# Performance work log

Measured on AMD Instinct MI355X. Metric: run time of the kernel, lower is better.

Reference implementation:

```python
import jax, jax.numpy as jnp
import numpy as np

N_NODES = 100000
N_EDGES = 6400000
EPS = 1e-12


def _gcn_conv(x, edge_index, W, b, n):
    # PyG GCNConv(normalize=True): add self-loops, symmetric deg^-1/2 norm
    src, dst = edge_index[0], edge_index[1]
    loop = jnp.arange(n)
    row = jnp.concatenate([src, loop])
    col = jnp.concatenate([dst, loop])
    deg = jax.ops.segment_sum(jnp.ones(row.shape[0], dtype=x.dtype), col, num_segments=n)
    dinv = jnp.where(deg > 0, jax.lax.rsqrt(deg), 0.0)
    norm = dinv[row] * dinv[col]                       # [E+N]
    xw = x @ W                                          # [N,16]
    out = jax.ops.segment_sum(xw[row] * norm[:, None], col, num_segments=n)
    return out + b


def _sage_conv(x, edge_index, Wl, bl, Wr, n):
    # PyG SAGEConv(aggr='mean', root_weight=True, normalize=True)
    src, dst = edge_index[0], edge_index[1]
    deg = jax.ops.segment_sum(jnp.ones(src.shape[0], dtype=x.dtype), dst, num_segments=n)
    agg = jax.ops.segment_sum(x[src], dst, num_segments=n) / jnp.maximum(deg, 1.0)[:, None]
    out = agg @ Wl + bl + x @ Wr
    nrm = jnp.sqrt(jnp.sum(out * out, axis=-1, keepdims=True))
    return out / jnp.maximum(nrm, EPS)                  # F.normalize(p=2)


def setup_inputs() -> dict:
    key = jax.random.key(0)
    ks = jax.random.split(key, 16)
    s16, s128 = 1.0 / np.sqrt(16.0), 1.0 / np.sqrt(128.0)
    inp = {
        "x": jax.random.normal(ks[0], (N_NODES, 16), dtype=jnp.float32),
        "edge_index": jax.random.randint(ks[1], (2, N_EDGES), 0, N_NODES, dtype=jnp.int64),
        "W_gcn": jax.random.uniform(ks[2], (16, 16), jnp.float32, -s16, s16),
        "b_gcn": jnp.zeros((16,), jnp.float32),
        "Wl1": jax.random.uniform(ks[3], (16, 16), jnp.float32, -s16, s16),
        "bl1": jnp.zeros((16,), jnp.float32),
        "Wr1": jax.random.uniform(ks[4], (16, 16), jnp.float32, -s16, s16),
        "Wl2": jax.random.uniform(ks[5], (16, 16), jnp.float32, -s16, s16),
        "bl2": jnp.zeros((16,), jnp.float32),
        "Wr2": jax.random.uniform(ks[6], (16, 16), jnp.float32, -s16, s16),
        "W1": jax.random.uniform(ks[7], (16, 128), jnp.float32, -s16, s16),
        "b1": jax.random.uniform(ks[8], (128,), jnp.float32, -s16, s16),
        "W2": jax.random.uniform(ks[9], (128, 128), jnp.float32, -s128, s128),
        "b2": jax.random.uniform(ks[10], (128,), jnp.float32, -s128, s128),
        "W3": jax.random.uniform(ks[11], (128, 1), jnp.float32, -s128, s128),
        "b3": jax.random.uniform(ks[12], (1,), jnp.float32, -s128, s128),
    }
    return inp


def reference(x, edge_index, W_gcn, b_gcn, Wl1, bl1, Wr1, Wl2, bl2, Wr2, W1, b1, W2, b2, W3, b3):
    n = x.shape[0]
    h = jnp.tanh(_gcn_conv(x, edge_index, W_gcn, b_gcn, n))
    h = jnp.tanh(_sage_conv(h, edge_index, Wl1, bl1, Wr1, n))
    h = _sage_conv(h, edge_index, Wl2, bl2, Wr2, n)
    h = jax.nn.relu(h @ W1 + b1)
    h = jax.nn.relu(h @ W2 + b2)
    return h @ W3 + b3
```

## Files before the change

kernel.cpp:

```cpp
#include <hip/hip_runtime.h>
#include <hip/hip_bf16.h>
#include <math.h>

#define NBLK 512
#define ROWS (NBLK / 256)
#define MAXNC 512
#define STAGE_CAP 12512

__global__ void k_hist(const int* __restrict__ dst, int* __restrict__ hist,
                       int nE, int nc, int chunk) {
    __shared__ int ch[MAXNC];
    int b = blockIdx.x, t = threadIdx.x;
    for (int i = t; i < nc; i += 256) ch[i] = 0;
    __syncthreads();
    int c0 = b * chunk, c1 = min(nE, c0 + chunk);
    if (c1 > c0) {
        int nv = (c1 - c0) >> 2;
        const int4* d4 = (const int4*)(dst + c0);
        for (int i = t; i < nv; i += 256) {
            int4 dd = d4[i];
            atomicAdd(&ch[dd.x >> 8], 1);
            atomicAdd(&ch[dd.y >> 8], 1);
            atomicAdd(&ch[dd.z >> 8], 1);
            atomicAdd(&ch[dd.w >> 8], 1);
        }
        int rem = (c1 - c0) & 3;
        if (t < rem) atomicAdd(&ch[dst[c0 + (nv << 2) + t] >> 8], 1);
    }
    __syncthreads();
    for (int i = t; i < nc; i += 256) hist[b * nc + i] = ch[i];
}

__global__ void k_scanA(const int* __restrict__ hist, int* __restrict__ offT,
                        int* __restrict__ totPad, int* __restrict__ totReal, int nc) {
    __shared__ int sums[256];
    __shared__ int red[256];
    int c = blockIdx.x, t = threadIdx.x;
    int v[ROWS], p[ROWS];
    int s = 0, sr = 0;
#pragma unroll
    for (int j = 0; j < ROWS; ++j) {
        v[j] = hist[(size_t)(t * ROWS + j) * nc + c];
        p[j] = (v[j] + 15) & ~15;
        s += p[j];
        sr += v[j];
    }
    sums[t] = s;
    red[t] = sr;
    __syncthreads();
    for (int d = 1; d < 256; d <<= 1) {
        int x = (t >= d) ? sums[t - d] : 0;
        __syncthreads();
        sums[t] += x;
        __syncthreads();
    }
    int run = sums[t] - s;
#pragma unroll
    for (int j = 0; j < ROWS; ++j) {
        offT[(size_t)c * NBLK + t * ROWS + j] = run;
        run += p[j];
    }
    if (t == 255) totPad[c] = sums[255];
    for (int d = 128; d > 0; d >>= 1) {
        if (t < d) red[t] += red[t + d];
        __syncthreads();
    }
    if (t == 0) totReal[c] = red[0];
}

__global__ void k_scanB(const int* __restrict__ totPad, const int* __restrict__ totReal,
                        int* __restrict__ cbase, int* __restrict__ rbase,
                        int* __restrict__ rowstart, int nE, int nc, int n) {
    __shared__ int sp[512];
    __shared__ int sr[512];
    int t = threadIdx.x;
    int vp = (t < nc) ? totPad[t] : 0;
    int vr = (t < nc) ? totReal[t] : 0;
    sp[t] = vp; sr[t] = vr;
    __syncthreads();
    for (int d = 1; d < 512; d <<= 1) {
        int xp = (t >= d) ? sp[t - d] : 0;
        int xr = (t >= d) ? sr[t - d] : 0;
        __syncthreads();
        sp[t] += xp; sr[t] += xr;
        __syncthreads();
    }
    if (t < nc) { cbase[t] = sp[t] - vp; rbase[t] = sr[t] - vr; }
    if (t == nc - 1) cbase[nc] = sp[t];
    if (t == 0) rowstart[n] = nE;
}

__global__ __launch_bounds__(256, 2)
void k_fill(const int* __restrict__ src, const int* __restrict__ dst,
            const int* __restrict__ hist, const int* __restrict__ offT,
            const int* __restrict__ cbase,
            int* __restrict__ bucketed, int nE, int nc, int chunk) {
    __shared__ int stage[STAGE_CAP];
    __shared__ int sc[256];
    __shared__ int lbeg[MAXNC];
    __shared__ int lcur[MAXNC];
    int b = blockIdx.x, t = threadIdx.x;

    int v0 = (2 * t < nc) ? hist[(size_t)b * nc + 2 * t] : 0;
    int v1 = (2 * t + 1 < nc) ? hist[(size_t)b * nc + 2 * t + 1] : 0;
    int s = v0 + v1;
    sc[t] = s;
    __syncthreads();
    for (int d = 1; d < 256; d <<= 1) {
        int x = (t >= d) ? sc[t - d] : 0;
        __syncthreads();
        sc[t] += x;
        __syncthreads();
    }
    int excl = sc[t] - s;
    if (2 * t < nc) { lbeg[2 * t] = excl; lcur[2 * t] = excl; }
    if (2 * t + 1 < nc) { lbeg[2 * t + 1] = excl + v0; lcur[2 * t + 1] = excl + v0; }
    __syncthreads();

    int c0 = b * chunk, c1 = min(nE, c0 + chunk);
    if (c1 > c0) {
        int nv = (c1 - c0) >> 2;
        const int4* d4 = (const int4*)(dst + c0);
        const int4* s4 = (const int4*)(src + c0);
        for (int i = t; i < nv; i += 256) {
            int4 dd = d4[i];
            int4 ss = s4[i];
            int pos;
            pos = atomicAdd(&lcur[dd.x >> 8], 1); stage[pos] = ss.x | ((dd.x & 255) << 17);
            pos = atomicAdd(&lcur[dd.y >> 8], 1); stage[pos] = ss.y | ((dd.y & 255) << 17);
            pos = atomicAdd(&lcur[dd.z >> 8], 1); stage[pos] = ss.z | ((dd.z & 255) << 17);
            pos = atomicAdd(&lcur[dd.w >> 8], 1); stage[pos] = ss.w | ((dd.w & 255) << 17);
        }
        int rem = (c1 - c0) & 3;
        if (t < rem) {
            int e = c0 + (nv << 2) + t;
            int d = dst[e];
            int pos = atomicAdd(&lcur[d >> 8], 1);
            stage[pos] = src[e] | ((d & 255) << 17);
        }
    }
    __syncthreads();

    for (int c = t; c < nc; c += 256) {
        int lo = lbeg[c];
        int cnt = lcur[c] - lo;
        int g = cbase[c] + offT[(size_t)c * NBLK + b];
        int padded = (cnt + 15) & ~15;
        for (int i = 0; i < padded; i += 4) {
            int4 v;
            v.x = (i + 0 < cnt) ? stage[lo + i + 0] : -1;
            v.y = (i + 1 < cnt) ? stage[lo + i + 1] : -1;
            v.z = (i + 2 < cnt) ? stage[lo + i + 2] : -1;
            v.w = (i + 3 < cnt) ? stage[lo + i + 3] : -1;
            *(int4*)(bucketed + g + i) = v;
        }
    }
}

__global__ void k_fine(const int* __restrict__ bucketed, const int* __restrict__ cbase,
                       const int* __restrict__ rbase,
                       int* __restrict__ csr, int* __restrict__ rowstart,
                       float* __restrict__ dinv, int n) {
    __shared__ int cnt[256];
    __shared__ int lrs[512];
    __shared__ int cur[256];
    int cb = blockIdx.x, t = threadIdx.x;
    int e0 = cbase[cb], e1 = cbase[cb + 1];
    int r0 = rbase[cb];
    if (t < 256) cnt[t] = 0;
    __syncthreads();
    int nv = (e1 - e0) >> 2;
    const int4* b4 = (const int4*)(bucketed + e0);
    for (int i = t; i < nv; i += 512) {
        int4 en = b4[i];
        if (en.x >= 0) atomicAdd(&cnt[(en.x >> 17) & 255], 1);
        if (en.y >= 0) atomicAdd(&cnt[(en.y >> 17) & 255], 1);
        if (en.z >= 0) atomicAdd(&cnt[(en.z >> 17) & 255], 1);
        if (en.w >= 0) atomicAdd(&cnt[(en.w >> 17) & 255], 1);
    }
    __syncthreads();
    int my = (t < 256) ? cnt[t] : 0;
    lrs[t] = my;
    __syncthreads();
    for (int d = 1; d < 512; d <<= 1) {
        int x = (t >= d) ? lrs[t - d] : 0;
        __syncthreads();
        lrs[t] += x;
        __syncthreads();
    }
    if (t < 256) {
        int excl = lrs[t] - my;
        int node = cb * 256 + t;
        if (node < n) {
            rowstart[node] = r0 + excl;
            dinv[node] = rsqrtf((float)(my + 1));
        }
        cur[t] = r0 + excl;
    }
    __syncthreads();
    for (int i = t; i < nv; i += 512) {
        int4 en = b4[i];
        int pos;
        if (en.x >= 0) { pos = atomicAdd(&cur[(en.x >> 17) & 255], 1); csr[pos] = en.x & 0x1FFFF; }
        if (en.y >= 0) { pos = atomicAdd(&cur[(en.y >> 17) & 255], 1); csr[pos] = en.y & 0x1FFFF; }
        if (en.z >= 0) { pos = atomicAdd(&cur[(en.z >> 17) & 255], 1); csr[pos] = en.z & 0x1FFFF; }
        if (en.w >= 0) { pos = atomicAdd(&cur[(en.w >> 17) & 255], 1); csr[pos] = en.w & 0x1FFFF; }
    }
}

__global__ void k_prescale(const float* __restrict__ x, const float* __restrict__ dinv,
                           float* __restrict__ xs, int n) {
    int i = blockIdx.x * blockDim.x + threadIdx.x;
    if (i >= n) return;
    float di = dinv[i];
    const float4* xp = (const float4*)(x + (size_t)i * 16);
    float4* op = (float4*)(xs + (size_t)i * 16);
#pragma unroll
    for (int q = 0; q < 4; ++q) {
        float4 v = xp[q];
        v.x *= di; v.y *= di; v.z *= di; v.w *= di;
        op[q] = v;
    }
}

template <int MODE>
__global__ void k_conv(const float* __restrict__ hin, const int* __restrict__ csr,
                       const int* __restrict__ rowstart, const float* __restrict__ dinv,
                       const float* __restrict__ Wa, const float* __restrict__ ba,
                       const float* __restrict__ Wb,
                       float* __restrict__ hout, int n) {
    int wid = (blockIdx.x * blockDim.x + threadIdx.x) >> 6;
    if (wid >= n) return;
    int lane = threadIdx.x & 63;
    int q = lane >> 2;
    int c = lane & 3;
    int r0 = rowstart[wid], r1 = rowstart[wid + 1];
    int cnt = r1 - r0;
    const int* p = csr + r0 + q;
    int my = (cnt > q) ? ((cnt - q + 15) >> 4) : 0;

    float av[4] = {0.f, 0.f, 0.f, 0.f};
    int t = 0;
    for (; t + 4 <= my; t += 4) {
        int s0 = p[(t + 0) * 16];
        int s1 = p[(t + 1) * 16];
        int s2 = p[(t + 2) * 16];
        int s3 = p[(t + 3) * 16];
        float4 v0 = *(const float4*)(hin + (size_t)s0 * 16 + c * 4);
        float4 v1 = *(const float4*)(hin + (size_t)s1 * 16 + c * 4);
        float4 v2 = *(const float4*)(hin + (size_t)s2 * 16 + c * 4);
        float4 v3 = *(const float4*)(hin + (size_t)s3 * 16 + c * 4);
        av[0] += (v0.x + v1.x) + (v2.x + v3.x);
        av[1] += (v0.y + v1.y) + (v2.y + v3.y);
        av[2] += (v0.z + v1.z) + (v2.z + v3.z);
        av[3] += (v0.w + v1.w) + (v2.w + v3.w);
    }
    if (t + 2 <= my) {
        int s0 = p[(t + 0) * 16];
        int s1 = p[(t + 1) * 16];
        float4 v0 = *(const float4*)(hin + (size_t)s0 * 16 + c * 4);
        float4 v1 = *(const float4*)(hin + (size_t)s1 * 16 + c * 4);
        av[0] += v0.x + v1.x; av[1] += v0.y + v1.y;
        av[2] += v0.z + v1.z; av[3] += v0.w + v1.w;
        t += 2;
    }
    if (t < my) {
        int s0 = p[t * 16];
        float4 v0 = *(const float4*)(hin + (size_t)s0 * 16 + c * 4);
        av[0] += v0.x; av[1] += v0.y; av[2] += v0.z; av[3] += v0.w;
    }
#pragma unroll
    for (int m = 4; m <= 32; m <<= 1) {
#pragma unroll
        for (int j = 0; j < 4; ++j) av[j] += __shfl_xor(av[j], m);
    }

    float4 hv4 = *(const float4*)(hin + (size_t)wid * 16 + c * 4);
    float hvv[4] = {hv4.x, hv4.y, hv4.z, hv4.w};

    if (MODE == 0) {
        float di = dinv[wid];
#pragma unroll
        for (int j = 0; j < 4; ++j) av[j] = di * (av[j] + hvv[j]);
    } else {
        float inv = 1.0f / fmaxf((float)cnt, 1.0f);
#pragma unroll
        for (int j = 0; j < 4; ++j) av[j] *= inv;
    }

    int fo = lane & 15;
    float y = ba[fo];
#pragma unroll
    for (int k = 0; k < 16; ++k) {
        float ak = __shfl(av[k & 3], k >> 2);
        y += ak * Wa[k * 16 + fo];
        if (MODE != 0) {
            float hk = __shfl(hvv[k & 3], k >> 2);
            y += hk * Wb[k * 16 + fo];
        }
    }
    if (MODE == 0) {
        y = tanhf(y);
    } else {
        float sq = y * y;
        sq += __shfl_xor(sq, 1);
        sq += __shfl_xor(sq, 2);
        sq += __shfl_xor(sq, 4);
        sq += __shfl_xor(sq, 8);
        float nrm = fmaxf(sqrtf(sq), 1e-12f);
        y /= nrm;
        if (MODE == 1) y = tanhf(y);
    }
    if ((lane >> 4) == 0) hout[wid * 16 + fo] = y;
}

#define MLP_NODES 64
__global__ __launch_bounds__(256)
void k_mlp(const float* __restrict__ h3,
           const float* __restrict__ W1, const float* __restrict__ b1,
           const float* __restrict__ W2, const float* __restrict__ b2,
           const float* __restrict__ W3, const float* __restrict__ b3,
           float* __restrict__ out, int n) {
    __shared__ float t1T[128][65];
    __shared__ float hpart[MLP_NODES][5];

    int t = threadIdx.x;
    int w = t >> 6;
    int l = t & 63;
    int ow = __builtin_amdgcn_readfirstlane(w * 32);
    int node0 = blockIdx.x * MLP_NODES;
    int node = node0 + l;
    int nodec = min(node, n - 1);

    float acc[32];
    {
        float h[16];
        const float4* hp = (const float4*)(h3 + (size_t)nodec * 16);
#pragma unroll
        for (int q = 0; q < 4; ++q) {
            float4 v = hp[q];
            h[q * 4 + 0] = v.x; h[q * 4 + 1] = v.y; h[q * 4 + 2] = v.z; h[q * 4 + 3] = v.w;
        }
        const float* bp = b1 + ow;
#pragma unroll
        for (int j = 0; j < 32; ++j) acc[j] = bp[j];
#pragma unroll
        for (int k = 0; k < 16; ++k) {
            const float* wr = W1 + k * 128 + ow;
            float hk = h[k];
#pragma unroll
            for (int j = 0; j < 32; ++j) acc[j] += hk * wr[j];
        }
#pragma unroll
        for (int j = 0; j < 32; ++j) t1T[ow + j][l] = fmaxf(acc[j], 0.f);
    }
    __syncthreads();

    {
        const float* bp = b2 + ow;
#pragma unroll
        for (int j = 0; j < 32; ++j) acc[j] = bp[j];
    }
    for (int k = 0; k < 128; ++k) {
        float tk = t1T[k][l];
        const float* wr = W2 + k * 128 + ow;
#pragma unroll
        for (int j = 0; j < 32; ++j) acc[j] += tk * wr[j];
    }

    float part = 0.f;
    {
        const float* wr = W3 + ow;
#pragma unroll
        for (int j = 0; j < 32; ++j) part += fmaxf(acc[j], 0.f) * wr[j];
    }
    hpart[l][w] = part;
    __syncthreads();
    if (w == 0 && node < n) {
        out[node] = hpart[l][0] + hpart[l][1] + hpart[l][2] + hpart[l][3] + b3[0];
    }
}

extern "C" void kernel_launch(void* const* d_in, const int* in_sizes, int n_in,
                              void* d_out, int out_size, void* d_ws, size_t ws_size,
                              hipStream_t stream) {
    const float* x = (const float*)d_in[0];
    const int* ei = (const int*)d_in[1];
    const float* W_gcn = (const float*)d_in[2];
    const float* b_gcn = (const float*)d_in[3];
    const float* Wl1 = (const float*)d_in[4];
    const float* bl1 = (const float*)d_in[5];
    const float* Wr1 = (const float*)d_in[6];
    const float* Wl2 = (const float*)d_in[7];
    const float* bl2 = (const float*)d_in[8];
    const float* Wr2 = (const float*)d_in[9];
    const float* W1 = (const float*)d_in[10];
    const float* b1 = (const float*)d_in[11];
    const float* W2 = (const float*)d_in[12];
    const float* b2 = (const float*)d_in[13];
    const float* W3 = (const float*)d_in[14];
    const float* b3 = (const float*)d_in[15];

    const int N = in_sizes[0] / 16;
    const int E = in_sizes[1] / 2;
    const int NC = (N + 255) >> 8;
    const int chunk = (((E + NBLK - 1) / NBLK) + 3) & ~3;
    const int* src = ei;
    const int* dst = ei + E;

    char* w = (char*)d_ws;
    auto alloc = [&](size_t bytes) {
        void* p = (void*)w;
        w += (bytes + 255) & ~(size_t)255;
        return p;
    };
    int* hist = (int*)alloc((size_t)NBLK * NC * 4);
    int* offT = (int*)alloc((size_t)NBLK * NC * 4);
    int* totPad = (int*)alloc((size_t)NC * 4);
    int* totReal = (int*)alloc((size_t)NC * 4);
    int* cbase = (int*)alloc((size_t)(NC + 1) * 4);
    int* rbase = (int*)alloc((size_t)NC * 4);
    int* rowstart = (int*)alloc((size_t)(N + 1) * 4);
    float* dinv = (float*)alloc((size_t)N * 4);
    int* bucketed = (int*)alloc(((size_t)E + (size_t)NBLK * NC * 16) * 4);
    int* csr = (int*)alloc((size_t)E * 4);
    float* xs = (float*)alloc((size_t)N * 16 * 4);
    float* h1 = (float*)alloc((size_t)N * 16 * 4);
    float* h2 = (float*)alloc((size_t)N * 16 * 4);
    float* h3 = (float*)alloc((size_t)N * 16 * 4);

    k_hist<<<NBLK, 256, 0, stream>>>(dst, hist, E, NC, chunk);
    k_scanA<<<NC, 256, 0, stream>>>(hist, offT, totPad, totReal, NC);
    k_scanB<<<1, 512, 0, stream>>>(totPad, totReal, cbase, rbase, rowstart, E, NC, N);
    k_fill<<<NBLK, 256, 0, stream>>>(src, dst, hist, offT, cbase, bucketed, E, NC, chunk);
    k_fine<<<NC, 512, 0, stream>>>(bucketed, cbase, rbase, csr, rowstart, dinv, N);

    int blk = 256;
    int ngrid = (N + blk - 1) / blk;
    long long conv_threads = (long long)N * 64;
    int ggrid = (int)((conv_threads + blk - 1) / blk);

    k_prescale<<<ngrid, blk, 0, stream>>>(x, dinv, xs, N);
    k_conv<0><<<ggrid, blk, 0, stream>>>(xs, csr, rowstart, dinv, W_gcn, b_gcn, W_gcn, h1, N);
    k_conv<1><<<ggrid, blk, 0, stream>>>(h1, csr, rowstart, dinv, Wl1, bl1, Wr1, h2, N);
    k_conv<2><<<ggrid, blk, 0, stream>>>(h2, csr, rowstart, dinv, Wl2, bl2, Wr2, h3, N);

    int mgrid = (N + MLP_NODES - 1) / MLP_NODES;
    k_mlp<<<mgrid, blk, 0, stream>>>(h3, W1, b1, W2, b2, W3, b3, (float*)d_out, N);
}
```

Baseline: 332.7 us.

## Split conv into gather-aggregate kernel and separate dense post-transform kernel

Each graph conv layer is split into two kernels: k_agg does the per-node neighbor gather-sum (one wavefront per node) and writes the raw aggregate to a buffer, and k_post applies normalization, the 16x16 matmuls, L2 norm and tanh with 4 threads per node. This takes the per-node shuffle-heavy matmul epilogue off the latency-bound gather kernel, where only 16 of 64 lanes did useful work, and lets the epilogue use all lanes. In exchange it adds three extra launches and an extra write and read of an N x 16 aggregate buffer per layer.

```diff
diff --git a/kernel.cpp b/kernel.cpp
--- a/kernel.cpp
+++ b/kernel.cpp
@@ -223,12 +223,8 @@
     }
 }
 
-template <int MODE>
-__global__ void k_conv(const float* __restrict__ hin, const int* __restrict__ csr,
-                       const int* __restrict__ rowstart, const float* __restrict__ dinv,
-                       const float* __restrict__ Wa, const float* __restrict__ ba,
-                       const float* __restrict__ Wb,
-                       float* __restrict__ hout, int n) {
+__global__ void k_agg(const float* __restrict__ hin, const int* __restrict__ csr,
+                      const int* __restrict__ rowstart, float* __restrict__ agg, int n) {
     int wid = (blockIdx.x * blockDim.x + threadIdx.x) >> 6;
     if (wid >= n) return;
     int lane = threadIdx.x & 63;
@@ -238,6 +234,7 @@
     int cnt = r1 - r0;
     const int* p = csr + r0 + q;
     int my = (cnt > q) ? ((cnt - q + 15) >> 4) : 0;
+    const float4* hb = (const float4*)hin + c;
 
     float av[4] = {0.f, 0.f, 0.f, 0.f};
     int t = 0;
@@ -246,10 +243,10 @@
         int s1 = p[(t + 1) * 16];
         int s2 = p[(t + 2) * 16];
         int s3 = p[(t + 3) * 16];
-        float4 v0 = *(const float4*)(hin + (size_t)s0 * 16 + c * 4);
-        float4 v1 = *(const float4*)(hin + (size_t)s1 * 16 + c * 4);
-        float4 v2 = *(const float4*)(hin + (size_t)s2 * 16 + c * 4);
-        float4 v3 = *(const float4*)(hin + (size_t)s3 * 16 + c * 4);
+        float4 v0 = hb[(size_t)s0 * 4];
+        float4 v1 = hb[(size_t)s1 * 4];
+        float4 v2 = hb[(size_t)s2 * 4];
+        float4 v3 = hb[(size_t)s3 * 4];
         av[0] += (v0.x + v1.x) + (v2.x + v3.x);
         av[1] += (v0.y + v1.y) + (v2.y + v3.y);
         av[2] += (v0.z + v1.z) + (v2.z + v3.z);
@@ -258,15 +255,15 @@
     if (t + 2 <= my) {
         int s0 = p[(t + 0) * 16];
         int s1 = p[(t + 1) * 16];
-        float4 v0 = *(const float4*)(hin + (size_t)s0 * 16 + c * 4);
-        float4 v1 = *(const float4*)(hin + (size_t)s1 * 16 + c * 4);
+        float4 v0 = hb[(size_t)s0 * 4];
+        float4 v1 = hb[(size_t)s1 * 4];
         av[0] += v0.x + v1.x; av[1] += v0.y + v1.y;
         av[2] += v0.z + v1.z; av[3] += v0.w + v1.w;
         t += 2;
     }
     if (t < my) {
         int s0 = p[t * 16];
-        float4 v0 = *(const float4*)(hin + (size_t)s0 * 16 + c * 4);
+        float4 v0 = hb[(size_t)s0 * 4];
         av[0] += v0.x; av[1] += v0.y; av[2] += v0.z; av[3] += v0.w;
     }
 #pragma unroll
@@ -274,44 +271,83 @@
 #pragma unroll
         for (int j = 0; j < 4; ++j) av[j] += __shfl_xor(av[j], m);
     }
-
-    float4 hv4 = *(const float4*)(hin + (size_t)wid * 16 + c * 4);
-    float hvv[4] = {hv4.x, hv4.y, hv4.z, hv4.w};
-
+    if (q == 0)
+        *(float4*)(agg + (size_t)wid * 16 + c * 4) = make_float4(av[0], av[1], av[2], av[3]);
+}
+
+template <int MODE>
+__global__ void k_post(const float* __restrict__ agg, const float* __restrict__ hin,
+                       const int* __restrict__ rowstart, const float* __restrict__ dinv,
+                       const float* __restrict__ Wa, const float* __restrict__ ba,
+                       const float* __restrict__ Wb,
+                       float* __restrict__ hout, int n) {
+    int idx = blockIdx.x * blockDim.x + threadIdx.x;
+    int node = idx >> 2;
+    if (node >= n) return;
+    int t4 = idx & 3;
+    int lane = threadIdx.x & 63;
+    int lbase = lane & 60;
+
+    float4 av = *(const float4*)(agg + (size_t)node * 16 + t4 * 4);
+    float4 sv = *(const float4*)(hin + (size_t)node * 16 + t4 * 4);
+
+    float a[16], s[16];
+#pragma unroll
+    for (int g = 0; g < 4; ++g) {
+        a[g * 4 + 0] = __shfl(av.x, lbase + g);
+        a[g * 4 + 1] = __shfl(av.y, lbase + g);
+        a[g * 4 + 2] = __shfl(av.z, lbase + g);
+        a[g * 4 + 3] = __shfl(av.w, lbase + g);
+        s[g * 4 + 0] = __shfl(sv.x, lbase + g);
+        s[g * 4 + 1] = __shfl(sv.y, lbase + g);
+        s[g * 4 + 2] = __shfl(sv.z, lbase + g);
+        s[g * 4 + 3] = __shfl(sv.w, lbase + g);
+    }
+
+    int fo = t4 * 4;
+    float yv[4];
     if (MODE == 0) {
-        float di = dinv[wid];
-#pragma unroll
-        for (int j = 0; j < 4; ++j) av[j] = di * (av[j] + hvv[j]);
+        float di = dinv[node];
+#pragma unroll
+        for (int k = 0; k < 16; ++k) a[k] = di * (a[k] + s[k]);
+#pragma unroll
+        for (int j = 0; j < 4; ++j) yv[j] = ba[fo + j];
+#pragma unroll
+        for (int k = 0; k < 16; ++k) {
+            float4 w = *(const float4*)(Wa + k * 16 + fo);
+            yv[0] += a[k] * w.x; yv[1] += a[k] * w.y;
+            yv[2] += a[k] * w.z; yv[3] += a[k] * w.w;
+        }
+#pragma unroll
+        for (int j = 0; j < 4; ++j) yv[j] = tanhf(yv[j]);
     } else {
+        int cnt = rowstart[node + 1] - rowstart[node];
         float inv = 1.0f / fmaxf((float)cnt, 1.0f);
 #pragma unroll
-        for (int j = 0; j < 4; ++j) av[j] *= inv;
-    }
-
-    int fo = lane & 15;
-    float y = ba[fo];
-#pragma unroll
-    for (int k = 0; k < 16; ++k) {
-        float ak = __shfl(av[k & 3], k >> 2);
-        y += ak * Wa[k * 16 + fo];
-        if (MODE != 0) {
-            float hk = __shfl(hvv[k & 3], k >> 2);
-            y += hk * Wb[k * 16 + fo];
-        }
-    }
-    if (MODE == 0) {
-        y = tanhf(y);
-    } else {
-        float sq = y * y;
+        for (int k = 0; k < 16; ++k) a[k] *= inv;
+#pragma unroll
+        for (int j = 0; j < 4; ++j) yv[j] = ba[fo + j];
+#pragma unroll
+        for (int k = 0; k < 16; ++k) {
+            float4 wa = *(const float4*)(Wa + k * 16 + fo);
+            float4 wb = *(const float4*)(Wb + k * 16 + fo);
+            yv[0] += a[k] * wa.x + s[k] * wb.x;
+            yv[1] += a[k] * wa.y + s[k] * wb.y;
+            yv[2] += a[k] * wa.z + s[k] * wb.z;
+            yv[3] += a[k] * wa.w + s[k] * wb.w;
+        }
+        float sq = yv[0] * yv[0] + yv[1] * yv[1] + yv[2] * yv[2] + yv[3] * yv[3];
         sq += __shfl_xor(sq, 1);
         sq += __shfl_xor(sq, 2);
-        sq += __shfl_xor(sq, 4);
-        sq += __shfl_xor(sq, 8);
         float nrm = fmaxf(sqrtf(sq), 1e-12f);
-        y /= nrm;
-        if (MODE == 1) y = tanhf(y);
-    }
-    if ((lane >> 4) == 0) hout[wid * 16 + fo] = y;
+#pragma unroll
+        for (int j = 0; j < 4; ++j) yv[j] /= nrm;
+        if (MODE == 1) {
+#pragma unroll
+            for (int j = 0; j < 4; ++j) yv[j] = tanhf(yv[j]);
+        }
+    }
+    *(float4*)(hout + (size_t)node * 16 + fo) = make_float4(yv[0], yv[1], yv[2], yv[3]);
 }
 
 #define MLP_NODES 64
@@ -425,6 +461,7 @@
     int* bucketed = (int*)alloc(((size_t)E + (size_t)NBLK * NC * 16) * 4);
     int* csr = (int*)alloc((size_t)E * 4);
     float* xs = (float*)alloc((size_t)N * 16 * 4);
+    float* agg = (float*)alloc((size_t)N * 16 * 4);
     float* h1 = (float*)alloc((size_t)N * 16 * 4);
     float* h2 = (float*)alloc((size_t)N * 16 * 4);
     float* h3 = (float*)alloc((size_t)N * 16 * 4);
@@ -437,13 +474,20 @@
 
     int blk = 256;
     int ngrid = (N + blk - 1) / blk;
-    long long conv_threads = (long long)N * 64;
-    int ggrid = (int)((conv_threads + blk - 1) / blk);
+    long long agg_threads = (long long)N * 64;
+    int agrid = (int)((agg_threads + blk - 1) / blk);
+    int pgrid = (int)(((long long)N * 4 + blk - 1) / blk);
 
     k_prescale<<<ngrid, blk, 0, stream>>>(x, dinv, xs, N);
-    k_conv<0><<<ggrid, blk, 0, stream>>>(xs, csr, rowstart, dinv, W_gcn, b_gcn, W_gcn, h1, N);
-    k_conv<1><<<ggrid, blk, 0, stream>>>(h1, csr, rowstart, dinv, Wl1, bl1, Wr1, h2, N);
-    k_conv<2><<<ggrid, blk, 0, stream>>>(h2, csr, rowstart, dinv, Wl2, bl2, Wr2, h3, N);
+
+    k_agg<<<agrid, blk, 0, stream>>>(xs, csr, rowstart, agg, N);
+    k_post<0><<<pgrid, blk, 0, stream>>>(agg, xs, rowstart, dinv, W_gcn, b_gcn, W_gcn, h1, N);
+
+    k_agg<<<agrid, blk, 0, stream>>>(h1, csr, rowstart, agg, N);
+    k_post<1><<<pgrid, blk, 0, stream>>>(agg, h1, rowstart, dinv, Wl1, bl1, Wr1, h2, N);
+
+    k_agg<<<agrid, blk, 0, stream>>>(h2, csr, rowstart, agg, N);
+    k_post<2><<<pgrid, blk, 0, stream>>>(agg, h2, rowstart, dinv, Wl2, bl2, Wr2, h3, N);
 
     int mgrid = (N + MLP_NODES - 1) / MLP_NODES;
     k_mlp<<<mgrid, blk, 0, stream>>>(h3, W1, b1, W2, b2, W3, b3, (float*)d_out, N);
```

New measurement: 335.2 us. About the same (+0.8%).
